# Optimization experiments

Hardware: AMD Instinct MI355X
Metric: run time of the kernel (lower is better)

## Reference

```python
import jax, jax.numpy as jnp
import numpy as np

B, C, M, T = 2, 512, 16, 128
H = 8
D = C // H  # 64, divisible by 4 for 2D RoPE
G = C // 4  # GroupNorm groups = 128
S = M * T


def group_norm(x, scale, bias, groups=G, eps=1e-5):
    b, c, m, t = x.shape
    xg = x.reshape(b, groups, c // groups, m, t)
    mu = xg.mean(axis=(2, 3, 4), keepdims=True)
    var = xg.var(axis=(2, 3, 4), keepdims=True)
    xn = ((xg - mu) * jax.lax.rsqrt(var + eps)).reshape(b, c, m, t)
    return xn * scale[None, :, None, None] + bias[None, :, None, None]


def dwsep_conv(x, dw, pw):
    # depthwise 3x3 (groups=C) then pointwise 1x1
    y = jax.lax.conv_general_dilated(
        x, dw, window_strides=(1, 1), padding='SAME',
        dimension_numbers=('NCHW', 'HWIO', 'NCHW'), feature_group_count=x.shape[1])
    return jnp.einsum('bcmt,cd->bdmt', y, pw)


def rope2d(x):
    # x: [B,H,M,T,D]; first D/2 dims rotated by freq index m, last D/2 by time index t
    d = x.shape[-1]
    dh = d // 2
    q = dh // 2
    inv = 1.0 / (10000.0 ** (jnp.arange(q, dtype=jnp.float32) / q))

    def rot(v, ang):
        h = v.shape[-1] // 2
        v1, v2 = v[..., :h], v[..., h:]
        c, s = jnp.cos(ang), jnp.sin(ang)
        return jnp.concatenate([v1 * c - v2 * s, v1 * s + v2 * c], axis=-1)

    ang_f = jnp.arange(x.shape[2], dtype=jnp.float32)[:, None] * inv  # [M,q]
    ang_t = jnp.arange(x.shape[3], dtype=jnp.float32)[:, None] * inv  # [T,q]
    xf = rot(x[..., :dh], ang_f[:, None, :])  # broadcast over T
    xt = rot(x[..., dh:], ang_t)
    return jnp.concatenate([xf, xt], axis=-1)


def setup_inputs() -> dict:
    key = jax.random.key(0)
    ks = jax.random.split(key, 14)
    s = 0.02
    return {
        'x': jax.random.normal(ks[0], (B, C, M, T), jnp.float32),
        'lengths': jax.random.randint(ks[1], (B,), T // 2, T + 1),
        'gn_scale': jnp.ones((C,), jnp.float32),
        'gn_bias': jnp.zeros((C,), jnp.float32),
        'dw_q': jax.random.normal(ks[2], (3, 3, 1, C), jnp.float32) * s,
        'dw_k': jax.random.normal(ks[3], (3, 3, 1, C), jnp.float32) * s,
        'dw_v': jax.random.normal(ks[4], (3, 3, 1, C), jnp.float32) * s,
        'pw_q': jax.random.normal(ks[5], (C, C), jnp.float32) * s,
        'pw_k': jax.random.normal(ks[6], (C, C), jnp.float32) * s,
        'pw_v': jax.random.normal(ks[7], (C, C), jnp.float32) * s,
        'attn_w': jax.random.normal(ks[8], (C, C), jnp.float32) * s,
        'attn_b': jnp.zeros((C,), jnp.float32),
        'out_w': jax.random.normal(ks[9], (C, C), jnp.float32) * s,
        'out_b': jnp.zeros((C,), jnp.float32),
    }


def reference(x, lengths, gn_scale, gn_bias, dw_q, dw_k, dw_v, pw_q, pw_k, pw_v,
              attn_w, attn_b, out_w, out_b):
    residual = x
    xn = group_norm(x, gn_scale, gn_bias)

    def to_heads(y):  # [B,C,M,T] -> [B,H,M,T,D]
        return y.reshape(B, H, D, M, T).transpose(0, 1, 3, 4, 2)

    q = rope2d(to_heads(dwsep_conv(xn, dw_q, pw_q)))
    k = rope2d(to_heads(dwsep_conv(xn, dw_k, pw_k)))
    v = to_heads(dwsep_conv(xn, dw_v, pw_v))

    q = q.reshape(B, H, S, D)
    k = k.reshape(B, H, S, D)
    v = v.reshape(B, H, S, D)

    scores = jnp.einsum('bhsd,bhkd->bhsk', q, k) / np.sqrt(D).astype(np.float32)
    valid_t = jnp.arange(T)[None, :] < lengths[:, None]        # [B,T]
    valid = jnp.tile(valid_t, (1, M))                          # [B,S], token idx = m*T + t
    scores = jnp.where(valid[:, None, None, :], scores, jnp.float32(-1e9))
    attn = jax.nn.softmax(scores, axis=-1)
    o = jnp.einsum('bhsk,bhkd->bhsd', attn, v)                 # [B,H,S,D]

    o = o.transpose(0, 2, 1, 3).reshape(B, S, C)
    o = o @ attn_w + attn_b                                    # block output proj
    o = o.reshape(B, M, T, C).transpose(0, 3, 1, 2)            # [B,C,M,T]
    out = jnp.einsum('bcmt,cd->bdmt', o, out_w) + out_b[None, :, None, None]
    return residual + out
```

## Files before the change

kernel.cpp:

```cpp
#include <hip/hip_runtime.h>
#include <math.h>

#define CCH 512
#define SSQ 2048
#define MTOT 4096

typedef __bf16 bf16;
typedef __bf16 bf16x8 __attribute__((ext_vector_type(8)));
typedef __bf16 bf16x4 __attribute__((ext_vector_type(4)));
typedef float  f32x4  __attribute__((ext_vector_type(4)));

#define AS1 __attribute__((address_space(1)))
#define AS3 __attribute__((address_space(3)))
__device__ __forceinline__ void glds16(const void* g, void* l) {
    __builtin_amdgcn_global_load_lds((const AS1 void*)g, (AS3 void*)l, 16, 0, 0);
}

__global__ __launch_bounds__(256) void gnw_kernel(const float* __restrict__ x,
        float* __restrict__ mu, float* __restrict__ rstd,
        const float* __restrict__ w0, const float* __restrict__ w1,
        const float* __restrict__ w2, const float* __restrict__ w3,
        const float* __restrict__ w4, bf16* __restrict__ wT) {
    __shared__ float smem[64*65];
    int tid = threadIdx.x;
    if (blockIdx.x < 256) {
        float* s_sum = smem;
        float* s_sq  = smem + 256;
        int bg = blockIdx.x;
        long base = (long)bg * 8192;
        float sum = 0.f, sq = 0.f;
#pragma unroll
        for (int r = 0; r < 32; ++r) {
            float v = x[base + r*256 + tid];
            sum += v; sq += v*v;
        }
        s_sum[tid] = sum; s_sq[tid] = sq;
        __syncthreads();
        for (int off = 128; off > 0; off >>= 1) {
            if (tid < off) { s_sum[tid] += s_sum[tid+off]; s_sq[tid] += s_sq[tid+off]; }
            __syncthreads();
        }
        if (tid == 0) {
            float m = s_sum[0] * (1.f/8192.f);
            float v = s_sq[0]  * (1.f/8192.f) - m*m;
            mu[bg] = m;
            rstd[bg] = rsqrtf(v + 1e-5f);
        }
    } else {
        int bid = blockIdx.x - 256;
        int z = bid >> 6, r2 = bid & 63;
        int k0 = (r2 >> 3)*64, n0 = (r2 & 7)*64;
        const float* srcs[5] = {w0, w1, w2, w3, w4};
        const float* W = srcs[z];
        bf16* D = wT + (long)z * (CCH*CCH);
        float (*t)[65] = (float(*)[65])smem;
        int cI = tid & 63, r4 = tid >> 6;
#pragma unroll
        for (int p = 0; p < 16; ++p) {
            int kr = p*4 + r4;
            t[kr][cI] = W[(long)(k0+kr)*CCH + n0 + cI];
        }
        __syncthreads();
#pragma unroll
        for (int p = 0; p < 16; ++p) {
            int nr = p*4 + r4;
            D[(long)(n0+nr)*CCH + k0 + cI] = (bf16)t[cI][nr];
        }
    }
}

__global__ void tn_kernel(const float* __restrict__ x, const float* __restrict__ mu,
                          const float* __restrict__ rstd, const float* __restrict__ gsc,
                          const float* __restrict__ gbs, bf16* __restrict__ xnT) {
    __shared__ float t[64][65];
    int s0 = blockIdx.x*64, c0 = blockIdx.y*64, b = blockIdx.z;
    int tid = threadIdx.x;
    int cI = tid & 63, r4 = tid >> 6;
#pragma unroll
    for (int p = 0; p < 16; ++p) {
        int cr = p*4 + r4;
        t[cr][cI] = x[((long)(b*CCH + c0 + cr))*SSQ + s0 + cI];
    }
    __syncthreads();
#pragma unroll
    for (int p = 0; p < 16; ++p) {
        int sr = p*4 + r4;
        int c = c0 + cI;
        int g = b*128 + (c >> 2);
        float v = (t[cI][sr] - mu[g]) * rstd[g] * gsc[c] + gbs[c];
        xnT[((long)(b*SSQ + s0 + sr))*CCH + c] = (bf16)v;
    }
}

__global__ __launch_bounds__(256) void dw3_kernel(const bf16* __restrict__ xnT,
        const float* __restrict__ dwq, const float* __restrict__ dwk,
        const float* __restrict__ dwv,
        bf16* __restrict__ yq, bf16* __restrict__ yk, bf16* __restrict__ yv) {
    int tid = threadIdx.x;
    int cc = (tid & 63) * 8;
    int s  = blockIdx.x*4 + (tid >> 6);
    int sl = s & (SSQ-1);
    int b  = s >> 11;
    int m = sl >> 7, t = sl & 127;
    float aq[8] = {}, ak[8] = {}, av[8] = {};
#pragma unroll
    for (int di = 0; di < 3; ++di) {
        int m2 = m + di - 1;
        if ((unsigned)m2 >= 16u) continue;
#pragma unroll
        for (int dj = 0; dj < 3; ++dj) {
            int t2 = t + dj - 1;
            if ((unsigned)t2 >= 128u) continue;
            bf16x8 xv = *(const bf16x8*)(xnT + ((long)(b*SSQ + m2*128 + t2))*CCH + cc);
            int wi = (di*3 + dj)*CCH + cc;
#pragma unroll
            for (int i = 0; i < 8; ++i) {
                float xf = (float)xv[i];
                aq[i] += xf * dwq[wi+i];
                ak[i] += xf * dwk[wi+i];
                av[i] += xf * dwv[wi+i];
            }
        }
    }
    bf16x8 oq, ok, ov;
#pragma unroll
    for (int i = 0; i < 8; ++i) { oq[i] = (bf16)aq[i]; ok[i] = (bf16)ak[i]; ov[i] = (bf16)av[i]; }
    long o = (long)s*CCH + cc;
    *(bf16x8*)(yq + o) = oq;
    *(bf16x8*)(yk + o) = ok;
    *(bf16x8*)(yv + o) = ov;
}

__device__ __forceinline__ void gemm_core64(const bf16* __restrict__ A,
        const bf16* __restrict__ Wt, int m0, int n0,
        char* As0, char* Bs0, f32x4 acc[2][2]) {
    int tid = threadIdx.x, lane = tid & 63, wid = tid >> 6;
    int sw = wid & 1, nw = wid >> 1;
    int col = lane & 15, quad = lane >> 4;
    const char* gA[2]; const char* gB[2]; int lo[2];
#pragma unroll
    for (int p = 0; p < 2; ++p) {
        int idx = tid + p*256;
        int row = idx >> 3;
        int c = (idx & 7) ^ (row & 7);
        gA[p] = (const char*)A  + ((long)(m0+row)*CCH + c*8)*2;
        gB[p] = (const char*)Wt + ((long)(n0+row)*CCH + c*8)*2;
        lo[p] = idx*16;
    }
    int rowA = sw*32 + col, rowB = nw*32 + col;
#pragma unroll
    for (int p = 0; p < 2; ++p) { glds16(gA[p], As0 + lo[p]); glds16(gB[p], Bs0 + lo[p]); }
#pragma unroll
    for (int it = 0; it < 8; ++it) {
        __syncthreads();
        if (it < 7) {
            int k2 = (it+1)*128;
            char* An = As0 + ((it+1)&1)*8192;
            char* Bn = Bs0 + ((it+1)&1)*8192;
#pragma unroll
            for (int p = 0; p < 2; ++p) { glds16(gA[p]+k2, An+lo[p]); glds16(gB[p]+k2, Bn+lo[p]); }
        }
        const char* Ab = As0 + (it&1)*8192;
        const char* Bb = Bs0 + (it&1)*8192;
        bf16x8 af[2][2], bfr[2][2];
#pragma unroll
        for (int mt = 0; mt < 2; ++mt) {
            int r = rowA + mt*16;
#pragma unroll
            for (int ks = 0; ks < 2; ++ks) {
                int c = (ks*4 + quad) ^ (r & 7);
                af[mt][ks] = *(const bf16x8*)(Ab + r*128 + c*16);
            }
        }
#pragma unroll
        for (int nt = 0; nt < 2; ++nt) {
            int r = rowB + nt*16;
#pragma unroll
            for (int ks = 0; ks < 2; ++ks) {
                int c = (ks*4 + quad) ^ (r & 7);
                bfr[nt][ks] = *(const bf16x8*)(Bb + r*128 + c*16);
            }
        }
#pragma unroll
        for (int ks = 0; ks < 2; ++ks)
#pragma unroll
            for (int mt = 0; mt < 2; ++mt)
#pragma unroll
                for (int nt = 0; nt < 2; ++nt)
                    acc[mt][nt] = __builtin_amdgcn_mfma_f32_16x16x32_bf16(
                        af[mt][ks], bfr[nt][ks], acc[mt][nt], 0,0,0);
    }
}

__global__ __launch_bounds__(256) void gemm_qkv(const bf16* __restrict__ Abase,
        const bf16* __restrict__ wT, bf16* __restrict__ qout,
        bf16* __restrict__ kout, bf16* __restrict__ vout) {
    __shared__ char As[2*8192];
    __shared__ char Bs[2*8192];
    int m0 = blockIdx.x*64, n0 = blockIdx.y*64, z = blockIdx.z;
    f32x4 acc[2][2] = {};
    gemm_core64(Abase + (long)z*MTOT*CCH, wT + (long)z*CCH*CCH, m0, n0, As, Bs, acc);
    int tid = threadIdx.x, lane = tid & 63, wid = tid >> 6;
    int sw = wid & 1, nw = wid >> 1;
    int col = lane & 15, quad = lane >> 4;
    int nb = n0 + nw*32, mb = m0 + sw*32;
    if (z < 2) {
        bf16* outp = z ? kout : qout;
        float invf = __expf(-(float)col * 0.5756462732485114f);
        bool tHalf = (nb & 32) != 0;
        const float sc = z ? 1.0f : 0.125f;
#pragma unroll
        for (int st = 0; st < 2; ++st)
#pragma unroll
            for (int r = 0; r < 4; ++r) {
                int row = mb + st*16 + quad*4 + r;
                int sl = row & (SSQ-1);
                float pos = tHalf ? (float)(sl & 127) : (float)(sl >> 7);
                float ang = pos * invf;
                float sn, cs;
                __sincosf(ang, &sn, &cs);
                float x1 = acc[st][0][r], x2 = acc[st][1][r];
                outp[(long)row*CCH + nb + col]      = (bf16)((x1*cs - x2*sn)*sc);
                outp[(long)row*CCH + nb + 16 + col] = (bf16)((x1*sn + x2*cs)*sc);
            }
    } else {
#pragma unroll
        for (int st = 0; st < 2; ++st)
#pragma unroll
            for (int nt = 0; nt < 2; ++nt) {
                int n = nb + nt*16 + col;
                int row0 = mb + st*16 + quad*4;
                int b = row0 >> 11, sl0 = row0 & (SSQ-1);
                bf16x4 pk;
#pragma unroll
                for (int r = 0; r < 4; ++r) pk[r] = (bf16)acc[st][nt][r];
                *(bf16x4*)(vout + ((long)(b*CCH + n))*SSQ + sl0) = pk;
            }
    }
}

template<int MODE>
__global__ __launch_bounds__(256) void gemm_bf16(const bf16* __restrict__ A,
        const bf16* __restrict__ Wt, const float* __restrict__ bias,
        const float* __restrict__ resid, void* __restrict__ outv) {
    __shared__ char As[2*8192];
    __shared__ char Bs[2*8192];
    int m0 = blockIdx.x*64, n0 = blockIdx.y*64;
    f32x4 acc[2][2] = {};
    gemm_core64(A, Wt, m0, n0, As, Bs, acc);
    int tid = threadIdx.x, lane = tid & 63, wid = tid >> 6;
    int sw = wid & 1, nw = wid >> 1;
    int col = lane & 15, quad = lane >> 4;
    int nb = n0 + nw*32, mb = m0 + sw*32;
    if (MODE == 3) {
        bf16* outp = (bf16*)outv;
#pragma unroll
        for (int nt = 0; nt < 2; ++nt) {
            int n = nb + nt*16 + col;
            float bv = bias[n];
#pragma unroll
            for (int st = 0; st < 2; ++st)
#pragma unroll
                for (int r = 0; r < 4; ++r)
                    outp[(long)(mb + st*16 + quad*4 + r)*CCH + n] = (bf16)(acc[st][nt][r] + bv);
        }
    } else {
        float* outp = (float*)outv;
#pragma unroll
        for (int st = 0; st < 2; ++st)
#pragma unroll
            for (int nt = 0; nt < 2; ++nt) {
                int n = nb + nt*16 + col;
                float bv = bias[n];
                int row0 = mb + st*16 + quad*4;
                int b = row0 >> 11, sl0 = row0 & (SSQ-1);
                long off = ((long)(b*CCH + n))*SSQ + sl0;
                float4 rr = *(const float4*)(resid + off);
                float4 o4;
                o4.x = acc[st][nt][0] + bv + rr.x;
                o4.y = acc[st][nt][1] + bv + rr.y;
                o4.z = acc[st][nt][2] + bv + rr.z;
                o4.w = acc[st][nt][3] + bv + rr.w;
                *(float4*)(outp + off) = o4;
            }
    }
}

__global__ __launch_bounds__(256) void attn_kernel(
        const bf16* __restrict__ qb, const bf16* __restrict__ kb,
        const bf16* __restrict__ vb, const int* __restrict__ lengths,
        bf16* __restrict__ po0, bf16* __restrict__ po1,
        float* __restrict__ pl0, float* __restrict__ pl1) {
    __shared__ char KVs[16384];
    __shared__ bf16 Ps[4][16*72];
    int b = blockIdx.z, h = blockIdx.y;
    int qblk = blockIdx.x >> 1, sp = blockIdx.x & 1;
    int tid = threadIdx.x, wid = tid >> 6, lane = tid & 63;
    int col = lane & 15, quad = lane >> 4;
    int q0 = qblk*64 + wid*16;
    int lenb = lengths[b];

    const char* gp[4]; long gstep[4]; int ldsoff[4];
#pragma unroll
    for (int p = 0; p < 4; ++p) {
        int idx = tid + p*256;
        int isV = idx >> 9;
        int rem = idx & 511;
        int r = rem >> 3;
        int csrc = (rem & 7) ^ (r & 7);
        if (!isV) {
            gp[p] = (const char*)kb + ((long)(b*SSQ + sp*1024 + r))*1024 + h*128 + csrc*16;
            gstep[p] = 65536;
        } else {
            gp[p] = (const char*)vb + ((long)(b*CCH + h*64 + r))*4096 + sp*2048 + csrc*16;
            gstep[p] = 128;
        }
        ldsoff[p] = idx*16;
    }

    f32x4 vm[2][4];
#pragma unroll
    for (int p2 = 0; p2 < 2; ++p2)
#pragma unroll
        for (int sub = 0; sub < 4; ++sub)
#pragma unroll
            for (int r = 0; r < 4; ++r)
                vm[p2][sub][r] = (p2*64 + sub*16 + quad*4 + r < lenb) ? 1.f : 0.f;

    const bf16* qp = qb + (long)(b*SSQ)*CCH + h*64;
    bf16x8 qf[2];
#pragma unroll
    for (int dc = 0; dc < 2; ++dc)
        qf[dc] = *(const bf16x8*)(qp + (long)(q0 + col)*CCH + dc*32 + quad*8);

    f32x4 of[4] = {};
    float lsum = 0.f;
    bf16* pw = Ps[wid];
    int cswz = col & 7;

    bf16x8 sreg[4];
#pragma unroll
    for (int p = 0; p < 4; ++p) sreg[p] = *(const bf16x8*)(gp[p]);

    for (int t = 0; t < 16; ++t) {
        __syncthreads();
#pragma unroll
        for (int p = 0; p < 4; ++p) *(bf16x8*)(KVs + ldsoff[p]) = sreg[p];
        __syncthreads();
        if (t < 15) {
#pragma unroll
            for (int p = 0; p < 4; ++p)
                sreg[p] = *(const bf16x8*)(gp[p] + (long)(t+1)*gstep[p]);
        }
        const char* K = KVs;
        const char* V = KVs + 8192;
        int par = t & 1;
        f32x4 acc[4] = {};
#pragma unroll
        for (int sub = 0; sub < 4; ++sub)
#pragma unroll
            for (int dc = 0; dc < 2; ++dc) {
                bf16x8 kf = *(const bf16x8*)(K + (sub*16 + col)*128 + ((dc*4+quad) ^ cswz)*16);
                acc[sub] = __builtin_amdgcn_mfma_f32_16x16x32_bf16(kf, qf[dc], acc[sub], 0,0,0);
            }
#pragma unroll
        for (int sub = 0; sub < 4; ++sub) {
            bf16x4 pk;
#pragma unroll
            for (int r = 0; r < 4; ++r) {
                float p = __expf(acc[sub][r]) * vm[par][sub][r];
                lsum += p;
                pk[r] = (bf16)p;
            }
            *(bf16x4*)(pw + col*72 + sub*16 + quad*4) = pk;
        }
#pragma unroll
        for (int ks = 0; ks < 2; ++ks) {
            bf16x8 pf = *(const bf16x8*)(pw + col*72 + ks*32 + quad*8);
#pragma unroll
            for (int dt = 0; dt < 4; ++dt) {
                bf16x8 vf = *(const bf16x8*)(V + (dt*16 + col)*128 + ((ks*4+quad) ^ cswz)*16);
                of[dt] = __builtin_amdgcn_mfma_f32_16x16x32_bf16(pf, vf, of[dt], 0,0,0);
            }
        }
    }
    lsum += __shfl_xor(lsum, 16);
    lsum += __shfl_xor(lsum, 32);
    bf16* po = sp ? po1 : po0;
    float* pl = sp ? pl1 : pl0;
    if (quad == 0) pl[(b*8 + h)*SSQ + q0 + col] = lsum;
    bf16* ob = po + ((long)(b*SSQ + q0))*CCH + h*64;
#pragma unroll
    for (int dt = 0; dt < 4; ++dt)
#pragma unroll
        for (int r = 0; r < 4; ++r)
            ob[(long)(quad*4 + r)*CCH + dt*16 + col] = (bf16)of[dt][r];
}

__global__ __launch_bounds__(256) void attn_combine(
        const bf16* __restrict__ po0, const bf16* __restrict__ po1,
        const float* __restrict__ pl0, const float* __restrict__ pl1,
        bf16* __restrict__ o) {
    int idx = blockIdx.x*256 + threadIdx.x;
    int cc = idx & 127;
    int s  = (idx >> 7) & (SSQ-1);
    int b  = idx >> 18;
    int h  = cc >> 4;
    int li = (b*8 + h)*SSQ + s;
    float inv = 1.f / (pl0[li] + pl1[li]);
    bf16x4 a = ((const bf16x4*)po0)[idx];
    bf16x4 c4 = ((const bf16x4*)po1)[idx];
    bf16x4 r;
#pragma unroll
    for (int i = 0; i < 4; ++i)
        r[i] = (bf16)(((float)a[i] + (float)c4[i]) * inv);
    ((bf16x4*)o)[idx] = r;
}

extern "C" void kernel_launch(void* const* d_in, const int* in_sizes, int n_in,
                              void* d_out, int out_size, void* d_ws, size_t ws_size,
                              hipStream_t stream) {
    const float* x        = (const float*)d_in[0];
    const int*   lengths  = (const int*)  d_in[1];
    const float* gn_scale = (const float*)d_in[2];
    const float* gn_bias  = (const float*)d_in[3];
    const float* dw_q     = (const float*)d_in[4];
    const float* dw_k     = (const float*)d_in[5];
    const float* dw_v     = (const float*)d_in[6];
    const float* pw_q     = (const float*)d_in[7];
    const float* pw_k     = (const float*)d_in[8];
    const float* pw_v     = (const float*)d_in[9];
    const float* attn_w   = (const float*)d_in[10];
    const float* attn_b   = (const float*)d_in[11];
    const float* out_w    = (const float*)d_in[12];
    const float* out_b    = (const float*)d_in[13];
    float* out = (float*)d_out;

    char* w = (char*)d_ws;
    float* mu   = (float*)w;
    float* rstd = (float*)(w + 1024);
    bf16* wT    = (bf16*)(w + 4096);
    bf16* wTa = wT + 3*CCH*CCH;
    bf16* wTo = wT + 4*CCH*CCH;
    bf16* xnT  = (bf16*)(w + 0x00300000);
    bf16* yT   = (bf16*)(w + 0x00700000);
    bf16* qbf  = (bf16*)(w + 0x01300000);
    bf16* kbf  = (bf16*)(w + 0x01700000);
    bf16* vbf  = (bf16*)(w + 0x01B00000);
    bf16* obf  = (bf16*)(w + 0x01F00000);
    bf16* tmpb = (bf16*)(w + 0x02300000);
    bf16*  po0 = (bf16*)(w + 0x00700000);
    bf16*  po1 = (bf16*)(w + 0x00B00000);
    float* pl0 = (float*)(w + 0x00300000);
    float* pl1 = (float*)(w + 0x00320000);

    gnw_kernel<<<576, 256, 0, stream>>>(x, mu, rstd, pw_q, pw_k, pw_v, attn_w, out_w, wT);
    tn_kernel<<<dim3(32,8,2), 256, 0, stream>>>(x, mu, rstd, gn_scale, gn_bias, xnT);
    dw3_kernel<<<MTOT/4, 256, 0, stream>>>(xnT, dw_q, dw_k, dw_v,
                                           yT, yT + (long)MTOT*CCH, yT + (long)2*MTOT*CCH);

    gemm_qkv<<<dim3(MTOT/64, CCH/64, 3), 256, 0, stream>>>(yT, wT, qbf, kbf, vbf);

    attn_kernel<<<dim3(64, 8, 2), 256, 0, stream>>>(qbf, kbf, vbf, lengths, po0, po1, pl0, pl1);
    attn_combine<<<2048, 256, 0, stream>>>(po0, po1, pl0, pl1, obf);

    dim3 gg(MTOT/64, CCH/64);
    gemm_bf16<3><<<gg, 256, 0, stream>>>(obf, wTa, attn_b, nullptr, tmpb);
    gemm_bf16<4><<<gg, 256, 0, stream>>>(tmpb, wTo, out_b, x, out);
}
```

Before: 172.2 us.

## Fold output projections into one GEMM and drop split-KV attention combine

Precomputes the product of attn_w and out_w, plus the combined bias, inside the prep kernel so that only one projection GEMM runs after attention. Attention now processes the full key range per block and normalizes in-kernel, removing the partial buffers and the separate combine kernel. This trades fewer launches and less intermediate traffic for less attention parallelism, a naive fp32 weight-product computed each call, and slightly different rounding from the folded bf16 weight.

```diff
diff --git a/kernel.cpp b/kernel.cpp
--- a/kernel.cpp
+++ b/kernel.cpp
@@ -16,18 +16,20 @@
     __builtin_amdgcn_global_load_lds((const AS1 void*)g, (AS3 void*)l, 16, 0, 0);
 }
 
-__global__ __launch_bounds__(256) void gnw_kernel(const float* __restrict__ x,
+__global__ __launch_bounds__(256) void prep_kernel(const float* __restrict__ x,
         float* __restrict__ mu, float* __restrict__ rstd,
         const float* __restrict__ w0, const float* __restrict__ w1,
-        const float* __restrict__ w2, const float* __restrict__ w3,
-        const float* __restrict__ w4, bf16* __restrict__ wT) {
+        const float* __restrict__ w2,
+        const float* __restrict__ attn_w, const float* __restrict__ out_w,
+        const float* __restrict__ attn_b, const float* __restrict__ out_b,
+        bf16* __restrict__ wT, float* __restrict__ biasc) {
     __shared__ float smem[64*65];
     int tid = threadIdx.x;
-    if (blockIdx.x < 256) {
+    int bid = blockIdx.x;
+    if (bid < 256) {
         float* s_sum = smem;
         float* s_sq  = smem + 256;
-        int bg = blockIdx.x;
-        long base = (long)bg * 8192;
+        long base = (long)bid * 8192;
         float sum = 0.f, sq = 0.f;
 #pragma unroll
         for (int r = 0; r < 32; ++r) {
@@ -43,14 +45,14 @@
         if (tid == 0) {
             float m = s_sum[0] * (1.f/8192.f);
             float v = s_sq[0]  * (1.f/8192.f) - m*m;
-            mu[bg] = m;
-            rstd[bg] = rsqrtf(v + 1e-5f);
-        }
-    } else {
-        int bid = blockIdx.x - 256;
-        int z = bid >> 6, r2 = bid & 63;
+            mu[bid] = m;
+            rstd[bid] = rsqrtf(v + 1e-5f);
+        }
+    } else if (bid < 448) {
+        int b2 = bid - 256;
+        int z = b2 >> 6, r2 = b2 & 63;
         int k0 = (r2 >> 3)*64, n0 = (r2 & 7)*64;
-        const float* srcs[5] = {w0, w1, w2, w3, w4};
+        const float* srcs[3] = {w0, w1, w2};
         const float* W = srcs[z];
         bf16* D = wT + (long)z * (CCH*CCH);
         float (*t)[65] = (float(*)[65])smem;
@@ -66,6 +68,31 @@
             int nr = p*4 + r4;
             D[(long)(n0+nr)*CCH + k0 + cI] = (bf16)t[cI][nr];
         }
+    } else if (bid < 576) {
+        int cbid = bid - 448;
+        int k0 = (cbid >> 3)*32, n0 = (cbid & 7)*64;
+        int n = n0 + (tid & 63);
+        int kbase = k0 + (tid >> 6)*8;
+        float acc[8] = {};
+        for (int c = 0; c < CCH; ++c) {
+            float ow = out_w[(long)c*CCH + n];
+#pragma unroll
+            for (int kk = 0; kk < 8; ++kk)
+                acc[kk] += attn_w[(long)(kbase+kk)*CCH + c] * ow;
+        }
+        bf16* Dc = wT + (long)3 * (CCH*CCH);
+#pragma unroll
+        for (int kk = 0; kk < 8; ++kk)
+            Dc[(long)n*CCH + kbase + kk] = (bf16)acc[kk];
+    } else {
+        float a1 = 0.f, a2 = 0.f;
+        for (int c = 0; c < CCH; ++c) {
+            float ab = attn_b[c];
+            a1 += ab * out_w[(long)c*CCH + tid];
+            a2 += ab * out_w[(long)c*CCH + tid + 256];
+        }
+        biasc[tid]       = a1 + out_b[tid];
+        biasc[tid + 256] = a2 + out_b[tid + 256];
     }
 }
 
@@ -239,10 +266,9 @@
     }
 }
 
-template<int MODE>
-__global__ __launch_bounds__(256) void gemm_bf16(const bf16* __restrict__ A,
+__global__ __launch_bounds__(256) void gemm_proj(const bf16* __restrict__ A,
         const bf16* __restrict__ Wt, const float* __restrict__ bias,
-        const float* __restrict__ resid, void* __restrict__ outv) {
+        const float* __restrict__ resid, float* __restrict__ outp) {
     __shared__ char As[2*8192];
     __shared__ char Bs[2*8192];
     int m0 = blockIdx.x*64, n0 = blockIdx.y*64;
@@ -252,52 +278,35 @@
     int sw = wid & 1, nw = wid >> 1;
     int col = lane & 15, quad = lane >> 4;
     int nb = n0 + nw*32, mb = m0 + sw*32;
-    if (MODE == 3) {
-        bf16* outp = (bf16*)outv;
+#pragma unroll
+    for (int st = 0; st < 2; ++st)
 #pragma unroll
         for (int nt = 0; nt < 2; ++nt) {
             int n = nb + nt*16 + col;
             float bv = bias[n];
-#pragma unroll
-            for (int st = 0; st < 2; ++st)
-#pragma unroll
-                for (int r = 0; r < 4; ++r)
-                    outp[(long)(mb + st*16 + quad*4 + r)*CCH + n] = (bf16)(acc[st][nt][r] + bv);
-        }
-    } else {
-        float* outp = (float*)outv;
-#pragma unroll
-        for (int st = 0; st < 2; ++st)
-#pragma unroll
-            for (int nt = 0; nt < 2; ++nt) {
-                int n = nb + nt*16 + col;
-                float bv = bias[n];
-                int row0 = mb + st*16 + quad*4;
-                int b = row0 >> 11, sl0 = row0 & (SSQ-1);
-                long off = ((long)(b*CCH + n))*SSQ + sl0;
-                float4 rr = *(const float4*)(resid + off);
-                float4 o4;
-                o4.x = acc[st][nt][0] + bv + rr.x;
-                o4.y = acc[st][nt][1] + bv + rr.y;
-                o4.z = acc[st][nt][2] + bv + rr.z;
-                o4.w = acc[st][nt][3] + bv + rr.w;
-                *(float4*)(outp + off) = o4;
-            }
-    }
+            int row0 = mb + st*16 + quad*4;
+            int b = row0 >> 11, sl0 = row0 & (SSQ-1);
+            long off = ((long)(b*CCH + n))*SSQ + sl0;
+            float4 rr = *(const float4*)(resid + off);
+            float4 o4;
+            o4.x = acc[st][nt][0] + bv + rr.x;
+            o4.y = acc[st][nt][1] + bv + rr.y;
+            o4.z = acc[st][nt][2] + bv + rr.z;
+            o4.w = acc[st][nt][3] + bv + rr.w;
+            *(float4*)(outp + off) = o4;
+        }
 }
 
 __global__ __launch_bounds__(256) void attn_kernel(
         const bf16* __restrict__ qb, const bf16* __restrict__ kb,
         const bf16* __restrict__ vb, const int* __restrict__ lengths,
-        bf16* __restrict__ po0, bf16* __restrict__ po1,
-        float* __restrict__ pl0, float* __restrict__ pl1) {
+        bf16* __restrict__ o) {
     __shared__ char KVs[16384];
     __shared__ bf16 Ps[4][16*72];
     int b = blockIdx.z, h = blockIdx.y;
-    int qblk = blockIdx.x >> 1, sp = blockIdx.x & 1;
     int tid = threadIdx.x, wid = tid >> 6, lane = tid & 63;
     int col = lane & 15, quad = lane >> 4;
-    int q0 = qblk*64 + wid*16;
+    int q0 = blockIdx.x*64 + wid*16;
     int lenb = lengths[b];
 
     const char* gp[4]; long gstep[4]; int ldsoff[4];
@@ -308,13 +317,8 @@
         int rem = idx & 511;
         int r = rem >> 3;
         int csrc = (rem & 7) ^ (r & 7);
-        if (!isV) {
-            gp[p] = (const char*)kb + ((long)(b*SSQ + sp*1024 + r))*1024 + h*128 + csrc*16;
-            gstep[p] = 65536;
-        } else {
-            gp[p] = (const char*)vb + ((long)(b*CCH + h*64 + r))*4096 + sp*2048 + csrc*16;
-            gstep[p] = 128;
-        }
+        if (!isV) { gp[p] = (const char*)kb + ((long)(b*SSQ + r))*1024 + h*128 + csrc*16; gstep[p] = 65536; }
+        else      { gp[p] = (const char*)vb + ((long)(b*CCH + h*64 + r))*4096 + csrc*16;  gstep[p] = 128; }
         ldsoff[p] = idx*16;
     }
 
@@ -342,12 +346,12 @@
 #pragma unroll
     for (int p = 0; p < 4; ++p) sreg[p] = *(const bf16x8*)(gp[p]);
 
-    for (int t = 0; t < 16; ++t) {
+    for (int t = 0; t < 32; ++t) {
         __syncthreads();
 #pragma unroll
         for (int p = 0; p < 4; ++p) *(bf16x8*)(KVs + ldsoff[p]) = sreg[p];
         __syncthreads();
-        if (t < 15) {
+        if (t < 31) {
 #pragma unroll
             for (int p = 0; p < 4; ++p)
                 sreg[p] = *(const bf16x8*)(gp[p] + (long)(t+1)*gstep[p]);
@@ -386,35 +390,16 @@
     }
     lsum += __shfl_xor(lsum, 16);
     lsum += __shfl_xor(lsum, 32);
-    bf16* po = sp ? po1 : po0;
-    float* pl = sp ? pl1 : pl0;
-    if (quad == 0) pl[(b*8 + h)*SSQ + q0 + col] = lsum;
-    bf16* ob = po + ((long)(b*SSQ + q0))*CCH + h*64;
+    float invl = 1.f / lsum;
+    float ir[4];
+#pragma unroll
+    for (int r = 0; r < 4; ++r) ir[r] = __shfl(invl, quad*4 + r);
+    bf16* ob = o + (long)(b*SSQ + q0)*CCH + h*64;
 #pragma unroll
     for (int dt = 0; dt < 4; ++dt)
 #pragma unroll
         for (int r = 0; r < 4; ++r)
-            ob[(long)(quad*4 + r)*CCH + dt*16 + col] = (bf16)of[dt][r];
-}
-
-__global__ __launch_bounds__(256) void attn_combine(
-        const bf16* __restrict__ po0, const bf16* __restrict__ po1,
-        const float* __restrict__ pl0, const float* __restrict__ pl1,
-        bf16* __restrict__ o) {
-    int idx = blockIdx.x*256 + threadIdx.x;
-    int cc = idx & 127;
-    int s  = (idx >> 7) & (SSQ-1);
-    int b  = idx >> 18;
-    int h  = cc >> 4;
-    int li = (b*8 + h)*SSQ + s;
-    float inv = 1.f / (pl0[li] + pl1[li]);
-    bf16x4 a = ((const bf16x4*)po0)[idx];
-    bf16x4 c4 = ((const bf16x4*)po1)[idx];
-    bf16x4 r;
-#pragma unroll
-    for (int i = 0; i < 4; ++i)
-        r[i] = (bf16)(((float)a[i] + (float)c4[i]) * inv);
-    ((bf16x4*)o)[idx] = r;
+            ob[(long)(quad*4 + r)*CCH + dt*16 + col] = (bf16)(of[dt][r] * ir[r]);
 }
 
 extern "C" void kernel_launch(void* const* d_in, const int* in_sizes, int n_in,
@@ -440,31 +425,24 @@
     float* mu   = (float*)w;
     float* rstd = (float*)(w + 1024);
     bf16* wT    = (bf16*)(w + 4096);
-    bf16* wTa = wT + 3*CCH*CCH;
-    bf16* wTo = wT + 4*CCH*CCH;
+    bf16* wTc   = wT + (long)3*CCH*CCH;
+    float* biasc = (float*)(w + 0x00280000);
     bf16* xnT  = (bf16*)(w + 0x00300000);
     bf16* yT   = (bf16*)(w + 0x00700000);
     bf16* qbf  = (bf16*)(w + 0x01300000);
     bf16* kbf  = (bf16*)(w + 0x01700000);
     bf16* vbf  = (bf16*)(w + 0x01B00000);
     bf16* obf  = (bf16*)(w + 0x01F00000);
-    bf16* tmpb = (bf16*)(w + 0x02300000);
-    bf16*  po0 = (bf16*)(w + 0x00700000);
-    bf16*  po1 = (bf16*)(w + 0x00B00000);
-    float* pl0 = (float*)(w + 0x00300000);
-    float* pl1 = (float*)(w + 0x00320000);
-
-    gnw_kernel<<<576, 256, 0, stream>>>(x, mu, rstd, pw_q, pw_k, pw_v, attn_w, out_w, wT);
+
+    prep_kernel<<<577, 256, 0, stream>>>(x, mu, rstd, pw_q, pw_k, pw_v,
+                                         attn_w, out_w, attn_b, out_b, wT, biasc);
     tn_kernel<<<dim3(32,8,2), 256, 0, stream>>>(x, mu, rstd, gn_scale, gn_bias, xnT);
     dw3_kernel<<<MTOT/4, 256, 0, stream>>>(xnT, dw_q, dw_k, dw_v,
                                            yT, yT + (long)MTOT*CCH, yT + (long)2*MTOT*CCH);
 
     gemm_qkv<<<dim3(MTOT/64, CCH/64, 3), 256, 0, stream>>>(yT, wT, qbf, kbf, vbf);
 
-    attn_kernel<<<dim3(64, 8, 2), 256, 0, stream>>>(qbf, kbf, vbf, lengths, po0, po1, pl0, pl1);
-    attn_combine<<<2048, 256, 0, stream>>>(po0, po1, pl0, pl1, obf);
-
-    dim3 gg(MTOT/64, CCH/64);
-    gemm_bf16<3><<<gg, 256, 0, stream>>>(obf, wTa, attn_b, nullptr, tmpb);
-    gemm_bf16<4><<<gg, 256, 0, stream>>>(tmpb, wTo, out_b, x, out);
-}
+    attn_kernel<<<dim3(SSQ/64, 8, 2), 256, 0, stream>>>(qbf, kbf, vbf, lengths, obf);
+
+    gemm_proj<<<dim3(MTOT/64, CCH/64), 256, 0, stream>>>(obf, wTc, biasc, x, out);
+}
```

Measured after the change: 206.6 us. 1.2x slower.
